# Kernel optimization log

Measured on AMD Instinct MI355X. Metric: run time of the kernel, lower is better.

## Reference

```python
import jax, jax.numpy as jnp
import numpy as np

KERNEL_MUL = 2.0
KERNEL_NUM = 5


def setup_inputs() -> dict:
    key = jax.random.key(0)
    k1, k2 = jax.random.split(key)
    source = jax.random.normal(k1, (4096, 512), dtype=jnp.float32)
    target = jax.random.normal(k2, (4096, 512), dtype=jnp.float32)
    return {"source": source, "target": target}


def reference(source, target):
    b = source.shape[0]
    total = jnp.concatenate([source, target], axis=0)  # [N, D]
    n = total.shape[0]
    # pairwise squared L2 via dot-product trick (same math as expand-subtract)
    sq = jnp.sum(total * total, axis=1)  # [N]
    L2 = sq[:, None] + sq[None, :] - 2.0 * (total @ total.T)  # [N, N]
    # bandwidth uses .data in torch -> constant w.r.t. grads
    bw = jax.lax.stop_gradient(jnp.sum(L2)) / (n * n - n)
    bw = bw / (KERNEL_MUL ** (KERNEL_NUM // 2))
    kernels = jnp.zeros_like(L2)
    for i in range(KERNEL_NUM):  # small fixed loop over bandwidths
        kernels = kernels + jnp.exp(-L2 / (bw * (KERNEL_MUL ** i)))
    XX = jnp.mean(kernels[:b, :b])
    YY = jnp.mean(kernels[b:, b:])
    XY = jnp.mean(kernels[:b, b:])
    YX = jnp.mean(kernels[b:, :b])
    return XX + YY - XY - YX
```

## Files before the change

### kernel.cpp

```cpp
#include <hip/hip_runtime.h>
#include <cstdint>
#include <cstddef>


#define D_DIM 512
#define B_ROWS 4096
#define N_ROWS 8192
#define NTILES 64
#define NBLK_MMD 2080
#define QPITCH 528

typedef __attribute__((ext_vector_type(4))) int i32x4;

__device__ inline float waveReduce(float v) {
    #pragma unroll
    for (int off = 32; off > 0; off >>= 1) v += __shfl_down(v, off, 64);
    return v;
}

__device__ inline int q8(float x) {
    int v = (int)rintf(x * 16.f);
    v = v > 127 ? 127 : v;
    v = v < -127 ? -127 : v;
    return v & 255;
}

__global__ __launch_bounds__(256) void k_rowstats(const float* __restrict__ src,
                                                  const float* __restrict__ tgt,
                                                  unsigned char* __restrict__ Tp,
                                                  float* __restrict__ sq,
                                                  int* __restrict__ sp,
                                                  unsigned int* __restrict__ tk) {
    if (blockIdx.x == 0 && threadIdx.x < 65)
        tk[threadIdx.x * 16] = 0u;

    __shared__ unsigned char Q[16 * QPITCH];
    int tid = threadIdx.x, wave = tid >> 6, lane = tid & 63;
    int rb = blockIdx.x;

    #pragma unroll
    for (int i = 0; i < 4; ++i) {
        int rl  = wave * 4 + i;
        int row = rb * 16 + rl;
        const float* base = (row < B_ROWS) ? (src + (size_t)row * D_DIM)
                                           : (tgt + (size_t)(row - B_ROWS) * D_DIM);
        float4 a = ((const float4*)base)[lane * 2];
        float4 b = ((const float4*)base)[lane * 2 + 1];
        uint2 o;
        o.x = (unsigned)(q8(a.x) | (q8(a.y) << 8) | (q8(a.z) << 16) | (q8(a.w) << 24));
        o.y = (unsigned)(q8(b.x) | (q8(b.y) << 8) | (q8(b.z) << 16) | (q8(b.w) << 24));
        *(uint2*)(Q + rl * QPITCH + lane * 8) = o;
        float s = a.x*a.x + a.y*a.y + a.z*a.z + a.w*a.w
                + b.x*b.x + b.y*b.y + b.z*b.z + b.w*b.w;
        s = waveReduce(s);
        if (lane == 0) sq[row] = s;
    }
    __syncthreads();

    int s0 = 0, s1 = 0;
    #pragma unroll
    for (int r = 0; r < 16; ++r) {
        unsigned short v = *(const unsigned short*)(Q + r * QPITCH + tid * 2);
        s0 += (int)(signed char)(v & 255);
        s1 += (int)(signed char)(v >> 8);
    }
    int gbase = (rb & 7) * 512 + tid * 2;
    atomicAdd(&sp[gbase],     s0);
    atomicAdd(&sp[gbase + 1], s1);

    int c = tid >> 3, idx = tid & 7;
    uint4 lo = *(const uint4*)(Q + (idx * 2)     * QPITCH + c * 16);
    uint4 hi = *(const uint4*)(Q + (idx * 2 + 1) * QPITCH + c * 16);
    unsigned char* gout = Tp + ((size_t)rb << 13) + c * 256 + idx * 32;
    *(uint4*)(gout)      = lo;
    *(uint4*)(gout + 16) = hi;
}

__global__ __launch_bounds__(512) void k_bw(const int* __restrict__ sp,
                                            const float* __restrict__ sq,
                                            float* __restrict__ c16out) {
    int t = threadIdx.x;
    int csum = 0;
    #pragma unroll
    for (int g = 0; g < 8; ++g) csum += sp[g * 512 + t];
    float cs = (float)csum * 0.0625f;
    float p = cs * cs;
    float ssq = 0.f;
    #pragma unroll
    for (int i = 0; i < 16; ++i) ssq += sq[t + i * 512];
    __shared__ float r8[8], q8s[8];
    float wp = waveReduce(p);
    float wq = waveReduce(ssq);
    if ((t & 63) == 0) { r8[t >> 6] = wp; q8s[t >> 6] = wq; }
    __syncthreads();
    if (t == 0) {
        double P = 0.0, Q = 0.0;
        #pragma unroll
        for (int i = 0; i < 8; ++i) { P += r8[i]; Q += q8s[i]; }
        double n = (double)N_ROWS;
        double sumL2 = 2.0 * n * Q - 2.0 * P;
        double bw = sumL2 / (n * n - n) / 4.0;
        c16out[0] = (float)(-1.4426950408889634 / (16.0 * bw));
    }
}

__global__ __launch_bounds__(256) void k_mmd(const unsigned char* __restrict__ Tp,
                                             const float* __restrict__ sq,
                                             const float* __restrict__ c16in,
                                             float* __restrict__ blockpart,
                                             float* __restrict__ out,
                                             unsigned int* __restrict__ tk) {
    int hwbid = (int)blockIdx.x;
    int bid = (hwbid & 7) * 260 + (hwbid >> 3);

    int rem = bid;
    int ti = 0, rowlen = NTILES;
    while (rem >= rowlen) { rem -= rowlen; rowlen--; ti++; }
    int tj = ti + rem;

    int tid  = threadIdx.x;
    int wave = tid >> 6;
    int lane = tid & 63;
    int waveM = (wave >> 1) * 64;
    int waveN = (wave & 1) * 64;
    int l15   = lane & 15;
    int quad  = lane >> 4;

    float c16 = c16in[0];
    float cgq = -2.f * c16 * (1.f / 256.f);

    __shared__ unsigned char ldsA[65536];
    const unsigned char* gA = Tp + ((size_t)ti << 16);
    const unsigned char* gB = Tp + ((size_t)tj << 16);
    #pragma unroll
    for (int i = 0; i < 16; ++i) {
        int o = (i * 256 + tid) * 16;
        __builtin_amdgcn_global_load_lds(
            (const __attribute__((address_space(1))) void*)(gA + o),
            (__attribute__((address_space(3))) void*)(ldsA + o), 16, 0, 0);
    }
    __syncthreads();

    i32x4 acc[4][4];
    #pragma unroll
    for (int mi = 0; mi < 4; ++mi)
        #pragma unroll
        for (int ni = 0; ni < 4; ++ni)
            acc[mi][ni] = (i32x4){0, 0, 0, 0};

    int arow = (wave >> 1) * 4;
    int brow = (wave & 1) * 4;
    #pragma unroll
    for (int kk = 0; kk < 8; ++kk) {
        int coff = (kk * 4 + quad) * 256 + l15 * 16;
        i32x4 af[4], bf[4];
        #pragma unroll
        for (int ni = 0; ni < 4; ++ni)
            bf[ni] = *(const i32x4*)(gB + (size_t)((brow + ni) * 8192 + coff));
        #pragma unroll
        for (int mi = 0; mi < 4; ++mi)
            af[mi] = *(const i32x4*)(ldsA + (arow + mi) * 8192 + coff);
        #pragma unroll
        for (int mi = 0; mi < 4; ++mi)
            #pragma unroll
            for (int ni = 0; ni < 4; ++ni)
                acc[mi][ni] = __builtin_amdgcn_mfma_i32_16x16x64_i8(
                    af[mi], bf[ni], acc[mi][ni], 0, 0, 0);
    }

    const float* sqA = sq + ti * 128;
    const float* sqB = sq + tj * 128;
    float trow16[16];
    #pragma unroll
    for (int mi = 0; mi < 4; ++mi)
        #pragma unroll
        for (int r = 0; r < 4; ++r)
            trow16[mi * 4 + r] = sqA[waveM + mi * 16 + quad * 4 + r] * c16;
    float tcol16[4];
    #pragma unroll
    for (int ni = 0; ni < 4; ++ni)
        tcol16[ni] = sqB[waveN + ni * 16 + l15] * c16;

    float psum = 0.f;
    if (ti != tj) {
        #pragma unroll
        for (int mi = 0; mi < 4; ++mi) {
            #pragma unroll
            for (int ni = 0; ni < 4; ++ni) {
                #pragma unroll
                for (int r = 0; r < 4; ++r) {
                    float g   = (float)acc[mi][ni][r];
                    float t16 = __builtin_fmaf(g, cgq, trow16[mi * 4 + r]) + tcol16[ni];
                    float e1  = __builtin_amdgcn_exp2f(t16);
                    float e2  = e1 * e1;
                    float e4  = e2 * e2;
                    float e8  = e4 * e4;
                    float e16 = e8 * e8;
                    psum += ((e1 + e2) + (e4 + e8)) + e16;
                }
            }
        }
    } else {
        #pragma unroll
        for (int mi = 0; mi < 4; ++mi) {
            #pragma unroll
            for (int ni = 0; ni < 4; ++ni) {
                #pragma unroll
                for (int r = 0; r < 4; ++r) {
                    float g   = (float)acc[mi][ni][r];
                    float t16 = __builtin_fmaf(g, cgq, trow16[mi * 4 + r]) + tcol16[ni];
                    float e1  = __builtin_amdgcn_exp2f(t16);
                    float e2  = e1 * e1;
                    float e4  = e2 * e2;
                    float e8  = e4 * e4;
                    float e16 = e8 * e8;
                    float ks5 = ((e1 + e2) + (e4 + e8)) + e16;
                    int rl = waveM + mi * 16 + quad * 4 + r;
                    int cl = waveN + ni * 16 + l15;
                    psum += (rl == cl) ? 5.0f : ks5;
                }
            }
        }
    }

    __syncthreads();
    float* red   = (float*)ldsA;
    int*   flagp = (int*)ldsA + 4;
    float w = waveReduce(psum);
    if (lane == 0) red[wave] = w;
    __syncthreads();
    if (tid == 0) {
        float tot   = red[0] + red[1] + red[2] + red[3];
        float sign  = ((ti < 32) == (tj < 32)) ? 1.f : -1.f;
        float scale = (ti == tj) ? sign : 2.f * sign;
        __hip_atomic_store(&blockpart[hwbid], tot * scale,
                           __ATOMIC_RELAXED, __HIP_MEMORY_SCOPE_AGENT);
        asm volatile("s_waitcnt vmcnt(0)" ::: "memory");
        unsigned g = (unsigned)hwbid & 63u;
        unsigned tgt = (g < 32u) ? 33u : 32u;
        unsigned prev = __hip_atomic_fetch_add(&tk[g * 16], 1u,
                            __ATOMIC_RELAXED, __HIP_MEMORY_SCOPE_AGENT);
        int last = 0;
        if (prev == tgt - 1u)
            last = (__hip_atomic_fetch_add(&tk[64 * 16], 1u,
                        __ATOMIC_RELAXED, __HIP_MEMORY_SCOPE_AGENT) == 63u);
        *flagp = last;
    }
    __syncthreads();
    if (!*flagp) return;

    float s = 0.f;
    for (int i = tid; i < NBLK_MMD; i += 256)
        s += __hip_atomic_load(&blockpart[i], __ATOMIC_RELAXED,
                               __HIP_MEMORY_SCOPE_AGENT);
    float ws = waveReduce(s);
    __syncthreads();
    if (lane == 0) red[wave] = ws;
    __syncthreads();
    if (tid == 0)
        out[0] = (red[0] + red[1] + red[2] + red[3]) * (1.f / (4096.f * 4096.f));
}

extern "C" void kernel_launch(void* const* d_in, const int* in_sizes, int n_in,
                              void* d_out, int out_size, void* d_ws, size_t ws_size,
                              hipStream_t stream) {
    const float* src = (const float*)d_in[0];
    const float* tgt = (const float*)d_in[1];

    uint8_t* ws = (uint8_t*)d_ws;
    unsigned char* Tp = (unsigned char*)ws;
    size_t off = 4194304;
    float* sq      = (float*)(ws + off); off += 32768;
    int*   sp      = (int*)  (ws + off); off += 16384;
    float* bp      = (float*)(ws + off); off += 8320;
    float* c16     = (float*)(ws + off); off += 64;
    unsigned int* tk = (unsigned int*)(ws + off);

    hipMemsetAsync(sp, 0, 16384, stream);
    k_rowstats<<<512, 256, 0, stream>>>(src, tgt, Tp, sq, sp, tk);
    k_bw      <<<1, 512, 0, stream>>>(sp, sq, c16);
    k_mmd     <<<NBLK_MMD, 256, 0, stream>>>(Tp, sq, c16, bp, (float*)d_out, tk);
}
```

Measured before the change: 112.8 us.

## Enlarge MMD output tile to 256x256 with 512-thread blocks

Doubles the tile edge of the upper-triangular pairwise Gram computation from 128 to 256 rows, so there are 528 blocks of 512 threads instead of 2080 blocks of 256. Each block stages a 128KB A panel in LDS and each wave computes a 128x64 sub-tile with 32 accumulators. The goal is fewer blocks, less duplicated B-panel global traffic, and less per-block overhead. In exchange, LDS use per block is much larger, which limits occupancy to about one block per CU, register pressure rises, and the smaller grid gives coarser load balance.

New measurement: 113.5 us. About the same (+0.6%).

```diff
diff --git a/kernel.cpp b/kernel.cpp
--- a/kernel.cpp
+++ b/kernel.cpp
@@ -6,8 +6,8 @@
 #define D_DIM 512
 #define B_ROWS 4096
 #define N_ROWS 8192
-#define NTILES 64
-#define NBLK_MMD 2080
+#define NT2 32
+#define NBLK2 528
 #define QPITCH 528
 
 typedef __attribute__((ext_vector_type(4))) int i32x4;
@@ -104,78 +104,74 @@
     }
 }
 
-__global__ __launch_bounds__(256) void k_mmd(const unsigned char* __restrict__ Tp,
+__global__ __launch_bounds__(512) void k_mmd(const unsigned char* __restrict__ Tp,
                                              const float* __restrict__ sq,
                                              const float* __restrict__ c16in,
                                              float* __restrict__ blockpart,
                                              float* __restrict__ out,
                                              unsigned int* __restrict__ tk) {
     int hwbid = (int)blockIdx.x;
-    int bid = (hwbid & 7) * 260 + (hwbid >> 3);
+    int bid = (hwbid & 7) * 66 + (hwbid >> 3);
 
     int rem = bid;
-    int ti = 0, rowlen = NTILES;
+    int ti = 0, rowlen = NT2;
     while (rem >= rowlen) { rem -= rowlen; rowlen--; ti++; }
     int tj = ti + rem;
 
     int tid  = threadIdx.x;
     int wave = tid >> 6;
     int lane = tid & 63;
-    int waveM = (wave >> 1) * 64;
-    int waveN = (wave & 1) * 64;
+    int wr   = wave >> 2;
+    int wc   = wave & 3;
+    int waveM = wr * 128;
+    int waveN = wc * 64;
     int l15   = lane & 15;
     int quad  = lane >> 4;
 
     float c16 = c16in[0];
     float cgq = -2.f * c16 * (1.f / 256.f);
 
-    __shared__ unsigned char ldsA[65536];
-    const unsigned char* gA = Tp + ((size_t)ti << 16);
-    const unsigned char* gB = Tp + ((size_t)tj << 16);
+    __shared__ unsigned char ldsA[131072];
+    const unsigned char* gA = Tp + ((size_t)ti << 17);
+    const unsigned char* gB = Tp + ((size_t)tj << 17);
     #pragma unroll
     for (int i = 0; i < 16; ++i) {
-        int o = (i * 256 + tid) * 16;
+        int o = (i * 512 + tid) * 16;
         __builtin_amdgcn_global_load_lds(
             (const __attribute__((address_space(1))) void*)(gA + o),
             (__attribute__((address_space(3))) void*)(ldsA + o), 16, 0, 0);
     }
     __syncthreads();
 
-    i32x4 acc[4][4];
-    #pragma unroll
-    for (int mi = 0; mi < 4; ++mi)
+    i32x4 acc[8][4];
+    #pragma unroll
+    for (int mi = 0; mi < 8; ++mi)
         #pragma unroll
         for (int ni = 0; ni < 4; ++ni)
             acc[mi][ni] = (i32x4){0, 0, 0, 0};
 
-    int arow = (wave >> 1) * 4;
-    int brow = (wave & 1) * 4;
+    int arow = wr * 8;
+    int brow = wc * 4;
     #pragma unroll
     for (int kk = 0; kk < 8; ++kk) {
         int coff = (kk * 4 + quad) * 256 + l15 * 16;
-        i32x4 af[4], bf[4];
+        i32x4 af[8], bf[4];
         #pragma unroll
         for (int ni = 0; ni < 4; ++ni)
             bf[ni] = *(const i32x4*)(gB + (size_t)((brow + ni) * 8192 + coff));
         #pragma unroll
-        for (int mi = 0; mi < 4; ++mi)
+        for (int mi = 0; mi < 8; ++mi)
             af[mi] = *(const i32x4*)(ldsA + (arow + mi) * 8192 + coff);
         #pragma unroll
-        for (int mi = 0; mi < 4; ++mi)
+        for (int mi = 0; mi < 8; ++mi)
             #pragma unroll
             for (int ni = 0; ni < 4; ++ni)
                 acc[mi][ni] = __builtin_amdgcn_mfma_i32_16x16x64_i8(
                     af[mi], bf[ni], acc[mi][ni], 0, 0, 0);
     }
 
-    const float* sqA = sq + ti * 128;
-    const float* sqB = sq + tj * 128;
-    float trow16[16];
-    #pragma unroll
-    for (int mi = 0; mi < 4; ++mi)
-        #pragma unroll
-        for (int r = 0; r < 4; ++r)
-            trow16[mi * 4 + r] = sqA[waveM + mi * 16 + quad * 4 + r] * c16;
+    const float* sqA = sq + ti * 256;
+    const float* sqB = sq + tj * 256;
     float tcol16[4];
     #pragma unroll
     for (int ni = 0; ni < 4; ++ni)
@@ -184,13 +180,17 @@
     float psum = 0.f;
     if (ti != tj) {
         #pragma unroll
-        for (int mi = 0; mi < 4; ++mi) {
+        for (int mi = 0; mi < 8; ++mi) {
+            float trow4[4];
+            #pragma unroll
+            for (int r = 0; r < 4; ++r)
+                trow4[r] = sqA[waveM + mi * 16 + quad * 4 + r] * c16;
             #pragma unroll
             for (int ni = 0; ni < 4; ++ni) {
                 #pragma unroll
                 for (int r = 0; r < 4; ++r) {
                     float g   = (float)acc[mi][ni][r];
-                    float t16 = __builtin_fmaf(g, cgq, trow16[mi * 4 + r]) + tcol16[ni];
+                    float t16 = __builtin_fmaf(g, cgq, trow4[r]) + tcol16[ni];
                     float e1  = __builtin_amdgcn_exp2f(t16);
                     float e2  = e1 * e1;
                     float e4  = e2 * e2;
@@ -202,13 +202,17 @@
         }
     } else {
         #pragma unroll
-        for (int mi = 0; mi < 4; ++mi) {
+        for (int mi = 0; mi < 8; ++mi) {
+            float trow4[4];
+            #pragma unroll
+            for (int r = 0; r < 4; ++r)
+                trow4[r] = sqA[waveM + mi * 16 + quad * 4 + r] * c16;
             #pragma unroll
             for (int ni = 0; ni < 4; ++ni) {
                 #pragma unroll
                 for (int r = 0; r < 4; ++r) {
                     float g   = (float)acc[mi][ni][r];
-                    float t16 = __builtin_fmaf(g, cgq, trow16[mi * 4 + r]) + tcol16[ni];
+                    float t16 = __builtin_fmaf(g, cgq, trow4[r]) + tcol16[ni];
                     float e1  = __builtin_amdgcn_exp2f(t16);
                     float e2  = e1 * e1;
                     float e4  = e2 * e2;
@@ -225,19 +229,21 @@
 
     __syncthreads();
     float* red   = (float*)ldsA;
-    int*   flagp = (int*)ldsA + 4;
+    int*   flagp = (int*)ldsA + 8;
     float w = waveReduce(psum);
     if (lane == 0) red[wave] = w;
     __syncthreads();
     if (tid == 0) {
-        float tot   = red[0] + red[1] + red[2] + red[3];
-        float sign  = ((ti < 32) == (tj < 32)) ? 1.f : -1.f;
+        float tot = 0.f;
+        #pragma unroll
+        for (int i = 0; i < 8; ++i) tot += red[i];
+        float sign  = ((ti < 16) == (tj < 16)) ? 1.f : -1.f;
         float scale = (ti == tj) ? sign : 2.f * sign;
         __hip_atomic_store(&blockpart[hwbid], tot * scale,
                            __ATOMIC_RELAXED, __HIP_MEMORY_SCOPE_AGENT);
         asm volatile("s_waitcnt vmcnt(0)" ::: "memory");
         unsigned g = (unsigned)hwbid & 63u;
-        unsigned tgt = (g < 32u) ? 33u : 32u;
+        unsigned tgt = (g < 16u) ? 9u : 8u;
         unsigned prev = __hip_atomic_fetch_add(&tk[g * 16], 1u,
                             __ATOMIC_RELAXED, __HIP_MEMORY_SCOPE_AGENT);
         int last = 0;
@@ -250,15 +256,19 @@
     if (!*flagp) return;
 
     float s = 0.f;
-    for (int i = tid; i < NBLK_MMD; i += 256)
+    for (int i = tid; i < NBLK2; i += 512)
         s += __hip_atomic_load(&blockpart[i], __ATOMIC_RELAXED,
                                __HIP_MEMORY_SCOPE_AGENT);
     float ws = waveReduce(s);
     __syncthreads();
     if (lane == 0) red[wave] = ws;
     __syncthreads();
-    if (tid == 0)
-        out[0] = (red[0] + red[1] + red[2] + red[3]) * (1.f / (4096.f * 4096.f));
+    if (tid == 0) {
+        float tot = 0.f;
+        #pragma unroll
+        for (int i = 0; i < 8; ++i) tot += red[i];
+        out[0] = tot * (1.f / (4096.f * 4096.f));
+    }
 }
 
 extern "C" void kernel_launch(void* const* d_in, const int* in_sizes, int n_in,
@@ -279,5 +289,5 @@
     hipMemsetAsync(sp, 0, 16384, stream);
     k_rowstats<<<512, 256, 0, stream>>>(src, tgt, Tp, sq, sp, tk);
     k_bw      <<<1, 512, 0, stream>>>(sp, sq, c16);
-    k_mmd     <<<NBLK_MMD, 256, 0, stream>>>(Tp, sq, c16, bp, (float*)d_out, tk);
-}
+    k_mmd     <<<NBLK2, 512, 0, stream>>>(Tp, sq, c16, bp, (float*)d_out, tk);
+}
```
